# Kernel optimization log

Hardware: AMD Instinct MI355X
Metric: run time of the kernel (lower is better)

Reference implementation:

```python
import jax, jax.numpy as jnp
import numpy as np

STRIDE = 15           # cfg.shm.dilation_kernel
PAD = STRIDE // 2
P = 1048576           # cfg.shm.max_n_pixel (static sparse-pixel budget)


def dilate(alpha):
    # mask = (0.01 < alpha < 0.99); then 15x15 max-pool, stride 1, pad 7 (same size)
    m = jnp.logical_and(alpha > 0.01, alpha < 0.99).astype(alpha.dtype)
    return jax.lax.reduce_window(
        m, -jnp.inf, jax.lax.max,
        (1, 1, STRIDE, STRIDE), (1, 1, 1, 1),
        [(0, 0), (0, 0), (PAD, PAD), (PAD, PAD)])


def setup_inputs() -> dict:
    key = jax.random.key(0)
    ks = jax.random.split(key, 8)
    d = 128
    return {
        'image': jax.random.normal(ks[0], (8, 3, 512, 512), jnp.float32),
        'lr_pred': jax.random.uniform(ks[1], (8, 1, 512, 512), jnp.float32),
        'W1': jax.random.normal(ks[2], (4, d), jnp.float32) * 0.5,
        'b1': jnp.zeros((d,), jnp.float32),
        'W2': jax.random.normal(ks[3], (d, d), jnp.float32) * (1.0 / np.sqrt(d)),
        'b2': jnp.zeros((d,), jnp.float32),
        'W3': jax.random.normal(ks[4], (d, 1), jnp.float32) * (1.0 / np.sqrt(d)),
        'b3': jnp.zeros((1,), jnp.float32),
    }


def reference(image, lr_pred, W1, b1, W2, b2, W3, b3):
    B, C, H, W = image.shape
    mask = dilate(lr_pred)                       # [B,1,H,W] dilated uncertainty mask

    # generate_sparse_inputs: cat(img, (lr_pred-0.5)/0.5) channels-last, gather where mask>0
    feat = jnp.concatenate([image, (lr_pred - 0.5) / 0.5], axis=1)  # [B,4,H,W]
    feat = feat.transpose(0, 2, 3, 1).reshape(-1, C + 1)            # [B*H*W, 4]
    mflat = mask.reshape(-1)                                        # [B*H*W]

    (idx,) = jnp.nonzero(mflat > 0, size=P, fill_value=0)           # static-size gather
    count = jnp.sum(mflat > 0)
    valid = (jnp.arange(P) < count).astype(feat.dtype)              # [P]

    # torch's generate_sparse_inputs runs under no_grad -> stop_gradient on gather
    x = jax.lax.stop_gradient(feat[idx])                            # [P,4]

    # stand-in sparse head (shm): per-pixel MLP with sigmoid alpha output
    h = jax.nn.relu(x @ W1 + b1)
    h = jax.nn.relu(h @ W2 + b2)
    pred = jax.nn.sigmoid(h @ W3 + b3)[:, 0]                        # [P]

    # scatter predictions back to dense grid; ungathered masked pixels keep lr_pred
    scattered = jnp.zeros_like(mflat).at[idx].add(pred * valid)
    covered = jnp.zeros_like(mflat).at[idx].add(valid)
    lrf = lr_pred.reshape(-1)
    dense = scattered + (1.0 - covered) * lrf

    # final blend: pred*mask + lr_pred*(1-mask)
    final = dense * mflat + lrf * (1.0 - mflat)
    return final.reshape(B, 1, H, W)
```

## Files before the change

### kernel.cpp

```cpp
#include <hip/hip_runtime.h>
#include <hip/hip_bf16.h>
#include <math.h>

#define BB 8
#define HH 512
#define WW 512
#define NPIX (BB * HH * WW)
#define HWPIX (HH * WW)
#define PBUD 1048576
#define RAD 7
#define NB (NPIX / 256)
#define NMLP (NPIX / 128)

typedef __attribute__((ext_vector_type(4))) float f32x4;
typedef __attribute__((ext_vector_type(8))) short short8;
typedef __attribute__((ext_vector_type(4))) unsigned int u32x4;

__device__ __forceinline__ unsigned short f2bf(float f) {
    unsigned int u = __float_as_uint(f);
    unsigned int r = (u + 0x7fffu + ((u >> 16) & 1u)) >> 16;
    return (unsigned short)r;
}

__device__ __forceinline__ unsigned int pkbf(float a, float b) {
    __hip_bfloat162 h = __float22bfloat162_rn(make_float2(a, b));
    return *(unsigned int*)&h;
}

__global__ void k_prep_w2(const float* __restrict__ w2, unsigned short* __restrict__ w2f) {
    int i = blockIdx.x * 256 + threadIdx.x;
    int e  = i & 7;
    int l  = (i >> 3) & 63;
    int ks = (i >> 9) & 3;
    int jc = i >> 11;
    int j = jc * 16 + (l & 15);
    int k = ks * 32 + ((l >> 4) & 3) * 8 + e;
    w2f[i] = f2bf(w2[k * 128 + j]);
}

__global__ void k_rowdil(const float* __restrict__ lr, unsigned char* __restrict__ rowdil) {
    int p = blockIdx.x * 256 + threadIdx.x;
    int w = p & (WW - 1);
    int row0 = p - w;
    int lo = w - RAD; if (lo < 0) lo = 0;
    int hi = w + RAD; if (hi > WW - 1) hi = WW - 1;
    unsigned char any = 0;
    for (int x = lo; x <= hi; ++x) {
        float v = lr[row0 + x];
        any |= (unsigned char)(v > 0.01f && v < 0.99f);
    }
    rowdil[p] = any;
}

__global__ void k_coldil(const unsigned char* __restrict__ rowdil,
                         unsigned char* __restrict__ dm,
                         unsigned char* __restrict__ rankb,
                         int* __restrict__ gsum) {
    int p = blockIdx.x * 256 + threadIdx.x;
    int h = (p >> 9) & (HH - 1);
    int lo = h - RAD; if (lo < 0) lo = 0;
    int hi = h + RAD; if (hi > HH - 1) hi = HH - 1;
    lo -= h; hi -= h;
    unsigned char any = 0;
    for (int d = lo; d <= hi; ++d) any |= rowdil[p + d * WW];
    dm[p] = any;

    unsigned long long bal = __ballot(any != 0);
    __shared__ int wsum[4];
    int lane = threadIdx.x & 63;
    int wid  = threadIdx.x >> 6;
    if (lane == 0) wsum[wid] = __popcll(bal);
    __syncthreads();
    int pre = __popcll(bal & ((1ull << lane) - 1ull));
    int woff = 0;
    for (int i = 0; i < wid; ++i) woff += wsum[i];
    rankb[p] = (unsigned char)(woff + pre);
    if (threadIdx.x == 0) gsum[blockIdx.x] = wsum[0] + wsum[1] + wsum[2] + wsum[3];
}

__global__ void k_scan(const int* __restrict__ gsum, int* __restrict__ goff) {
    __shared__ int tsum[1024];
    int t = threadIdx.x;
    int base = t * 8;
    int v[8];
    int s = 0;
#pragma unroll
    for (int i = 0; i < 8; ++i) { v[i] = gsum[base + i]; s += v[i]; }
    tsum[t] = s;
    __syncthreads();
    for (int off = 1; off < 1024; off <<= 1) {
        int x = tsum[t];
        int y = (t >= off) ? tsum[t - off] : 0;
        __syncthreads();
        tsum[t] = x + y;
        __syncthreads();
    }
    int run = (t == 0) ? 0 : tsum[t - 1];
#pragma unroll
    for (int i = 0; i < 8; ++i) { goff[base + i] = run; run += v[i]; }
}

__global__ __launch_bounds__(256, 4)
void k_mlp(const float* __restrict__ image, const float* __restrict__ lr,
           const float* __restrict__ w1, const float* __restrict__ b1,
           const unsigned short* __restrict__ w2f, const float* __restrict__ b2,
           const float* __restrict__ w3, const float* __restrict__ b3,
           const unsigned char* __restrict__ dm, const unsigned char* __restrict__ rankb,
           const int* __restrict__ goff, float* __restrict__ out) {
    __shared__ __align__(16) char lds[32768];
    __shared__ float part_l[4][128];
    __shared__ int s_any;
    int g  = blockIdx.x;
    int p0 = g * 128;
    int t  = threadIdx.x;
    int px = t & 127;
    int p  = p0 + px;

    if (t == 0) s_any = 0;
    __syncthreads();
    float lrv = lr[p];
    bool  sel = dm[p] && (goff[p >> 8] + (int)rankb[p] < PBUD);
    if (sel) s_any = 1;
    __syncthreads();
    if (!s_any) {
        if (t < 128) out[p] = lrv;
        return;
    }

    int w    = t >> 6;
    int l    = t & 63;
    int lr16 = l & 15;
    int lh   = l >> 4;

    const short8* wf = (const short8*)w2f;
    short8 bf[2][4];
#pragma unroll
    for (int jj = 0; jj < 2; ++jj)
#pragma unroll
        for (int ks = 0; ks < 4; ++ks)
            bf[jj][ks] = wf[((2 * w + jj) * 4 + ks) * 64 + l];
    float b2v[2], w3v[2];
#pragma unroll
    for (int jj = 0; jj < 2; ++jj) {
        b2v[jj] = b2[(2 * w + jj) * 16 + lr16];
        w3v[jj] = w3[(2 * w + jj) * 16 + lr16];
    }
    float b3v = b3[0];

    {
        int jh = __builtin_amdgcn_readfirstlane(t >> 7);
        size_t bimg = (size_t)(p >> 18) * 3 * HWPIX + (p & (HWPIX - 1));
        float x0 = image[bimg];
        float x1 = image[bimg + HWPIX];
        float x2 = image[bimg + 2 * HWPIX];
        float x3 = 2.0f * lrv - 1.0f;
#pragma unroll
        for (int jc8 = 0; jc8 < 8; ++jc8) {
            int jc = jh * 8 + jc8;
            float h[8];
#pragma unroll
            for (int e = 0; e < 8; ++e) {
                int j = jc * 8 + e;
                float a = b1[j];
                a = fmaf(x0, w1[j], a);
                a = fmaf(x1, w1[128 + j], a);
                a = fmaf(x2, w1[256 + j], a);
                a = fmaf(x3, w1[384 + j], a);
                h[e] = fmaxf(a, 0.0f);
            }
            u32x4 pk = { pkbf(h[0], h[1]), pkbf(h[2], h[3]),
                         pkbf(h[4], h[5]), pkbf(h[6], h[7]) };
            int a = (((px << 8) | (jc << 4))) ^ ((px & 15) << 4);
            *(u32x4*)(lds + a) = pk;
        }
    }
    __syncthreads();

#pragma unroll
    for (int mt = 0; mt < 8; ++mt) {
        short8 af[4];
#pragma unroll
        for (int ks = 0; ks < 4; ++ks) {
            int row = mt * 16 + lr16;
            int a = (((row << 8) | (ks << 6) | (lh << 4))) ^ ((row & 15) << 4);
            af[ks] = *(const short8*)(lds + a);
        }
        f32x4 a0 = (f32x4){b2v[0], b2v[0], b2v[0], b2v[0]};
        f32x4 a1 = (f32x4){b2v[1], b2v[1], b2v[1], b2v[1]};
#pragma unroll
        for (int ks = 0; ks < 4; ++ks) {
            a0 = __builtin_amdgcn_mfma_f32_16x16x32_bf16(af[ks], bf[0][ks], a0, 0, 0, 0);
            a1 = __builtin_amdgcn_mfma_f32_16x16x32_bf16(af[ks], bf[1][ks], a1, 0, 0, 0);
        }
#pragma unroll
        for (int r = 0; r < 4; ++r) {
            float part = fmaxf(a0[r], 0.f) * w3v[0] + fmaxf(a1[r], 0.f) * w3v[1];
            part += __shfl_xor(part, 1);
            part += __shfl_xor(part, 2);
            part += __shfl_xor(part, 4);
            part += __shfl_xor(part, 8);
            if (lr16 == 0) part_l[w][mt * 16 + lh * 4 + r] = part;
        }
    }
    __syncthreads();

    if (t < 128) {
        float s = b3v + part_l[0][t] + part_l[1][t] + part_l[2][t] + part_l[3][t];
        out[p] = sel ? (1.0f / (1.0f + __expf(-s))) : lrv;
    }
}

extern "C" void kernel_launch(void* const* d_in, const int* in_sizes, int n_in,
                              void* d_out, int out_size, void* d_ws, size_t ws_size,
                              hipStream_t stream) {
    const float* image = (const float*)d_in[0];
    const float* lr    = (const float*)d_in[1];
    const float* w1    = (const float*)d_in[2];
    const float* b1    = (const float*)d_in[3];
    const float* w2    = (const float*)d_in[4];
    const float* b2    = (const float*)d_in[5];
    const float* w3    = (const float*)d_in[6];
    const float* b3    = (const float*)d_in[7];
    float* out = (float*)d_out;

    char* ws = (char*)d_ws;
    unsigned char* rowdil = (unsigned char*)ws;
    unsigned char* dm     = (unsigned char*)(ws + (size_t)NPIX);
    unsigned char* rankb  = (unsigned char*)(ws + 2 * (size_t)NPIX);
    int* gsum             = (int*)(ws + 3 * (size_t)NPIX);
    int* goff             = (int*)(ws + 3 * (size_t)NPIX + NB * 4);
    unsigned short* w2f   = (unsigned short*)(ws + 3 * (size_t)NPIX + 2 * NB * 4);

    k_prep_w2<<<64, 256, 0, stream>>>(w2, w2f);
    k_rowdil <<<NPIX / 256, 256, 0, stream>>>(lr, rowdil);
    k_coldil <<<NB, 256, 0, stream>>>(rowdil, dm, rankb, gsum);
    k_scan   <<<1, 1024, 0, stream>>>(gsum, goff);
    k_mlp    <<<NMLP, 256, 0, stream>>>(image, lr, w1, b1, w2f, b2, w3, b3,
                                        dm, rankb, goff, out);
}
```

Baseline: 132.5 us.

## Split MLP across 8 waves by row tile and drop LDS partial-sum reduction

The MLP kernel now launches 512 threads per 128-pixel block. Layer-1 work is split four ways across the threads. In layer 2 each of the 8 waves owns a 16-row tile and loops over all output column tiles, so the cross-wave partial-sum buffer and the final barrier go away, and outputs are written straight from the shuffle-reduced lanes. The aim is more waves for latency hiding and fewer barriers. In exchange, each wave now streams the whole bf16 W2 from global/cache memory instead of holding a slice in registers, which raises cache traffic, and the output lanes re-read the mask and rank data.

```diff
diff --git a/kernel.cpp b/kernel.cpp
--- a/kernel.cpp
+++ b/kernel.cpp
@@ -100,7 +100,7 @@
     for (int i = 0; i < 8; ++i) { goff[base + i] = run; run += v[i]; }
 }
 
-__global__ __launch_bounds__(256, 4)
+__global__ __launch_bounds__(512, 6)
 void k_mlp(const float* __restrict__ image, const float* __restrict__ lr,
            const float* __restrict__ w1, const float* __restrict__ b1,
            const unsigned short* __restrict__ w2f, const float* __restrict__ b2,
@@ -108,7 +108,6 @@
            const unsigned char* __restrict__ dm, const unsigned char* __restrict__ rankb,
            const int* __restrict__ goff, float* __restrict__ out) {
     __shared__ __align__(16) char lds[32768];
-    __shared__ float part_l[4][128];
     __shared__ int s_any;
     int g  = blockIdx.x;
     int p0 = g * 128;
@@ -127,40 +126,20 @@
         return;
     }
 
-    int w    = t >> 6;
-    int l    = t & 63;
-    int lr16 = l & 15;
-    int lh   = l >> 4;
-
-    const short8* wf = (const short8*)w2f;
-    short8 bf[2][4];
-#pragma unroll
-    for (int jj = 0; jj < 2; ++jj)
-#pragma unroll
-        for (int ks = 0; ks < 4; ++ks)
-            bf[jj][ks] = wf[((2 * w + jj) * 4 + ks) * 64 + l];
-    float b2v[2], w3v[2];
-#pragma unroll
-    for (int jj = 0; jj < 2; ++jj) {
-        b2v[jj] = b2[(2 * w + jj) * 16 + lr16];
-        w3v[jj] = w3[(2 * w + jj) * 16 + lr16];
-    }
-    float b3v = b3[0];
-
     {
-        int jh = __builtin_amdgcn_readfirstlane(t >> 7);
+        int jq = __builtin_amdgcn_readfirstlane(t >> 7);
         size_t bimg = (size_t)(p >> 18) * 3 * HWPIX + (p & (HWPIX - 1));
         float x0 = image[bimg];
         float x1 = image[bimg + HWPIX];
         float x2 = image[bimg + 2 * HWPIX];
         float x3 = 2.0f * lrv - 1.0f;
 #pragma unroll
-        for (int jc8 = 0; jc8 < 8; ++jc8) {
-            int jc = jh * 8 + jc8;
+        for (int c = 0; c < 4; ++c) {
+            int jcI = jq * 4 + c;
             float h[8];
 #pragma unroll
             for (int e = 0; e < 8; ++e) {
-                int j = jc * 8 + e;
+                int j = jcI * 8 + e;
                 float a = b1[j];
                 a = fmaf(x0, w1[j], a);
                 a = fmaf(x1, w1[128 + j], a);
@@ -170,43 +149,60 @@
             }
             u32x4 pk = { pkbf(h[0], h[1]), pkbf(h[2], h[3]),
                          pkbf(h[4], h[5]), pkbf(h[6], h[7]) };
-            int a = (((px << 8) | (jc << 4))) ^ ((px & 15) << 4);
+            int a = (((px << 8) | (jcI << 4))) ^ ((px & 15) << 4);
             *(u32x4*)(lds + a) = pk;
         }
     }
     __syncthreads();
 
-#pragma unroll
-    for (int mt = 0; mt < 8; ++mt) {
-        short8 af[4];
-#pragma unroll
-        for (int ks = 0; ks < 4; ++ks) {
-            int row = mt * 16 + lr16;
-            int a = (((row << 8) | (ks << 6) | (lh << 4))) ^ ((row & 15) << 4);
-            af[ks] = *(const short8*)(lds + a);
+    int w    = t >> 6;
+    int l    = t & 63;
+    int lr16 = l & 15;
+    int lh   = l >> 4;
+    int rowbase = w * 16;
+
+    short8 af[4];
+#pragma unroll
+    for (int ks = 0; ks < 4; ++ks) {
+        int row = rowbase + lr16;
+        int a = (((row << 8) | (ks << 6) | (lh << 4))) ^ (lr16 << 4);
+        af[ks] = *(const short8*)(lds + a);
+    }
+
+    float part[4] = {0.f, 0.f, 0.f, 0.f};
+    const short8* wf = (const short8*)w2f;
+#pragma unroll
+    for (int jc = 0; jc < 8; ++jc) {
+        short8 bf[4];
+#pragma unroll
+        for (int ks = 0; ks < 4; ++ks) bf[ks] = wf[(jc * 4 + ks) * 64 + l];
+        float b2v = b2[jc * 16 + lr16];
+        float w3v = w3[jc * 16 + lr16];
+        f32x4 acc = (f32x4){b2v, b2v, b2v, b2v};
+#pragma unroll
+        for (int ks = 0; ks < 4; ++ks)
+            acc = __builtin_amdgcn_mfma_f32_16x16x32_bf16(af[ks], bf[ks], acc, 0, 0, 0);
+#pragma unroll
+        for (int r = 0; r < 4; ++r)
+            part[r] = fmaf(fmaxf(acc[r], 0.f), w3v, part[r]);
+    }
+
+    float b3v = b3[0];
+#pragma unroll
+    for (int r = 0; r < 4; ++r) {
+        float pr = part[r];
+        pr += __shfl_xor(pr, 1);
+        pr += __shfl_xor(pr, 2);
+        pr += __shfl_xor(pr, 4);
+        pr += __shfl_xor(pr, 8);
+        if (lr16 == 0) {
+            int row = rowbase + lh * 4 + r;
+            int pp = p0 + row;
+            float lrvp = lr[pp];
+            bool ss = dm[pp] && (goff[pp >> 8] + (int)rankb[pp] < PBUD);
+            float logit = b3v + pr;
+            out[pp] = ss ? (1.0f / (1.0f + __expf(-logit))) : lrvp;
         }
-        f32x4 a0 = (f32x4){b2v[0], b2v[0], b2v[0], b2v[0]};
-        f32x4 a1 = (f32x4){b2v[1], b2v[1], b2v[1], b2v[1]};
-#pragma unroll
-        for (int ks = 0; ks < 4; ++ks) {
-            a0 = __builtin_amdgcn_mfma_f32_16x16x32_bf16(af[ks], bf[0][ks], a0, 0, 0, 0);
-            a1 = __builtin_amdgcn_mfma_f32_16x16x32_bf16(af[ks], bf[1][ks], a1, 0, 0, 0);
-        }
-#pragma unroll
-        for (int r = 0; r < 4; ++r) {
-            float part = fmaxf(a0[r], 0.f) * w3v[0] + fmaxf(a1[r], 0.f) * w3v[1];
-            part += __shfl_xor(part, 1);
-            part += __shfl_xor(part, 2);
-            part += __shfl_xor(part, 4);
-            part += __shfl_xor(part, 8);
-            if (lr16 == 0) part_l[w][mt * 16 + lh * 4 + r] = part;
-        }
-    }
-    __syncthreads();
-
-    if (t < 128) {
-        float s = b3v + part_l[0][t] + part_l[1][t] + part_l[2][t] + part_l[3][t];
-        out[p] = sel ? (1.0f / (1.0f + __expf(-s))) : lrv;
     }
 }
 
@@ -235,6 +231,6 @@
     k_rowdil <<<NPIX / 256, 256, 0, stream>>>(lr, rowdil);
     k_coldil <<<NB, 256, 0, stream>>>(rowdil, dm, rankb, gsum);
     k_scan   <<<1, 1024, 0, stream>>>(gsum, goff);
-    k_mlp    <<<NMLP, 256, 0, stream>>>(image, lr, w1, b1, w2f, b2, w3, b3,
+    k_mlp    <<<NMLP, 512, 0, stream>>>(image, lr, w1, b1, w2f, b2, w3, b3,
                                         dm, rankb, goff, out);
 }
```

After: 154.2 us. 1.16x slower.
